# Performance work log

Hardware: AMD Instinct MI355X
Metric: run time of the kernel (lower is better)

Reference implementation:

```python
import math
import jax, jax.numpy as jnp
import numpy as np

B, CIN, COUT, K, T, S = 16, 512, 512, 3, 2048, 128


def setup_inputs() -> dict:
    key = jax.random.key(0)
    k1, k2, k3, k4 = jax.random.split(key, 4)
    x = jax.random.normal(k1, (B, CIN, T), dtype=jnp.float32)
    c_trg = jax.random.normal(k2, (B, S), dtype=jnp.float32)
    style_w = jax.random.normal(k3, (CIN, S), dtype=jnp.float32)  # EqualLinear weight (lr_mul=1)
    style_b = jnp.ones((CIN,), dtype=jnp.float32)  # bias_init=1
    conv_w = jax.random.normal(k4, (1, COUT, CIN, K), dtype=jnp.float32)
    return {"x": x, "c_trg": c_trg, "style_w": style_w, "style_b": style_b, "conv_w": conv_w}


def reference(x, c_trg, style_w, style_b, conv_w):
    b, cin, t = x.shape
    cout, k = conv_w.shape[1], conv_w.shape[3]
    lin_scale = 1.0 / math.sqrt(style_w.shape[1])  # EqualLinear scale, lr_mul=1
    # original forward calls style_linear twice -> s and b are the SAME value
    s = c_trg @ (style_w * lin_scale).T + style_b            # [B, Cin]
    s = s[:, None, :, None]                                   # [B, 1, Cin, 1]
    conv_scale = 1.0 / math.sqrt(cin * k ** 2)
    w = conv_scale * (conv_w * s + s)                         # [B, Cout, Cin, K]
    demod = jax.lax.rsqrt(jnp.sum(w * w, axis=(2, 3)) + 1e-8)  # [B, Cout]
    demod_mean = jnp.mean(w.reshape(b, cout, -1), axis=2)      # [B, Cout]
    w = (w - demod_mean[:, :, None, None]) * demod[:, :, None, None]
    pad = k // 2

    def conv1(xi, wi):  # xi [Cin, T], wi [Cout, Cin, K]
        return jax.lax.conv_general_dilated(
            xi[None], wi, window_strides=(1,), padding=[(pad, pad)],
            dimension_numbers=("NCH", "OIH", "NCH"))[0]

    out = jax.vmap(conv1)(x, w)  # [B, Cout, T]
    return out
```

## Files before the change

kernel.cpp:

```cpp
#include <hip/hip_runtime.h>
#include <hip/hip_bf16.h>
#include <stdint.h>

#define B_    16
#define CIN_  512
#define COUT_ 512
#define K_    3
#define T_    2048
#define S_    128
#define TP_   2064
#define CXP_  2050

#define LIN_SCALE  0.08838834764831845f
#define CONV_SCALE 0.014731391274719739f

typedef unsigned short u16;
typedef short s16x8 __attribute__((ext_vector_type(8)));
typedef float f32x4 __attribute__((ext_vector_type(4)));
typedef u16 u16x8 __attribute__((ext_vector_type(8)));

__device__ __forceinline__ u16 bf16r(float f) {
    uint32_t u = __float_as_uint(f);
    return (u16)((u + 0x7FFFu + ((u >> 16) & 1u)) >> 16);
}

#define GLDS16(gsrc, ldst) \
    __builtin_amdgcn_global_load_lds((__attribute__((address_space(1))) void*)(gsrc), \
                                     (__attribute__((address_space(3))) void*)(ldst), 16, 0, 0)

__global__ void k_style(const float* __restrict__ c_trg,
                        const float* __restrict__ style_w,
                        const float* __restrict__ style_b,
                        float* __restrict__ s_out) {
    int idx = blockIdx.x * 256 + threadIdx.x;
    int b = idx >> 9, i = idx & 511;
    const float4* c4 = reinterpret_cast<const float4*>(c_trg + b * S_);
    const float4* w4 = reinterpret_cast<const float4*>(style_w + (size_t)i * S_);
    float acc = 0.f;
#pragma unroll
    for (int j = 0; j < S_ / 4; ++j) {
        float4 a = c4[j], w = w4[j];
        acc += a.x * w.x + a.y * w.y + a.z * w.z + a.w * w.w;
    }
    s_out[idx] = acc * LIN_SCALE + style_b[i];
}

__global__ void k_wsum(const float* __restrict__ conv_w,
                       float* __restrict__ W1, float* __restrict__ W2) {
    int idx = blockIdx.x * 256 + threadIdx.x;
    const float* wr = conv_w + (size_t)idx * 3;
    float a0 = wr[0] + 1.f, a1 = wr[1] + 1.f, a2 = wr[2] + 1.f;
    W1[idx] = a0 + a1 + a2;
    W2[idx] = a0 * a0 + a1 * a1 + a2 * a2;
}

__global__ void k_stats2(const float* __restrict__ s,
                         const float* __restrict__ W1, const float* __restrict__ W2,
                         float* __restrict__ alpha, float* __restrict__ beta) {
    int bo = blockIdx.x;
    int b = bo >> 9, o = bo & 511;
    const float* sb = s + b * CIN_;
    const float* w1 = W1 + (size_t)o * CIN_;
    const float* w2 = W2 + (size_t)o * CIN_;
    int l = threadIdx.x;
    float sum = 0.f, sq = 0.f;
#pragma unroll
    for (int r = 0; r < 8; ++r) {
        float sv = sb[l + r * 64];
        sum += sv * w1[l + r * 64];
        sq  += sv * sv * w2[l + r * 64];
    }
#pragma unroll
    for (int off = 32; off; off >>= 1) { sum += __shfl_down(sum, off); sq += __shfl_down(sq, off); }
    if (l == 0) {
        float mean  = CONV_SCALE * sum * (1.0f / (CIN_ * K_));
        float demod = rsqrtf(CONV_SCALE * CONV_SCALE * sq + 1e-8f);
        alpha[bo] = demod * CONV_SCALE;
        beta[bo]  = demod * mean;
    }
}

__global__ void k_prep_w(const float* __restrict__ conv_w, u16* __restrict__ wpk) {
    int idx = blockIdx.x * 256 + threadIdx.x;
    int j    = idx & 7;
    int lane = (idx >> 3) & 63;
    int grp  = (idx >> 9) & 7;
    int rest = idx >> 12;
    int tap  = rest % 3;
    int so   = rest / 3;
    int step = so & 15, ob = so >> 4;
    int o = ob * 128 + grp * 16 + (lane & 15);
    int i = step * 32 + (lane >> 4) * 8 + j;
    wpk[idx] = bf16r(conv_w[((size_t)o * CIN_ + i) * 3 + tap]);
}

__global__ void k_ytrans(const float* __restrict__ x, const float* __restrict__ s,
                         u16* __restrict__ ybf,
                         float* __restrict__ cxp, float* __restrict__ cyp) {
    int t = blockIdx.x * 256 + threadIdx.x;
    int oct = blockIdx.y, b = blockIdx.z;
    const float* xb = x + ((size_t)(b * CIN_ + oct * 8)) * T_ + t;
    const float* sb = s + b * CIN_ + oct * 8;
    float ax = 0.f, ay = 0.f;
    u16x8 pv;
#pragma unroll
    for (int j = 0; j < 8; ++j) {
        float xv = xb[(size_t)j * T_];
        float yv = sb[j] * xv;
        ax += xv; ay += yv;
        pv[j] = bf16r(yv);
    }
    *(u16x8*)(ybf + (((size_t)(b * 64 + oct)) * TP_ + t + 8) * 8) = pv;
    atomicAdd(&cxp[b * CXP_ + t + 1], ax);
    atomicAdd(&cyp[b * CXP_ + t + 1], ay);
    if (blockIdx.x == 0 && threadIdx.x < 8) {
        u16x8 z = {0, 0, 0, 0, 0, 0, 0, 0};
        *(u16x8*)(ybf + (((size_t)(b * 64 + oct)) * TP_ + threadIdx.x) * 8) = z;
    }
    if (blockIdx.x == 7 && threadIdx.x >= 248) {
        u16x8 z = {0, 0, 0, 0, 0, 0, 0, 0};
        *(u16x8*)(ybf + (((size_t)(b * 64 + oct)) * TP_ + 2056 + (threadIdx.x - 248)) * 8) = z;
    }
}

__global__ __launch_bounds__(256) void k_conv(
    const u16* __restrict__ wpk, const u16* __restrict__ ybf,
    const float* __restrict__ alpha, const float* __restrict__ beta,
    const float* __restrict__ cxp, const float* __restrict__ cyp,
    float* __restrict__ out) {

    __shared__ __align__(16) char smem[33792];

    const int tid  = threadIdx.x;
    const int lane = tid & 63;
    const int w    = tid >> 6;
    const int wr   = w >> 1, wc = w & 1;
    const int t0   = blockIdx.x * 128;
    const int ob   = blockIdx.y;
    const int b    = blockIdx.z;

    f32x4 acc[4][4] = {};

    const char* wsrc  = (const char*)wpk + (size_t)(ob * 16) * 24576 + (w * 6) * 1024 + lane * 16;
    const char* ybase = (const char*)ybf + ((size_t)b * 64) * (TP_ * 16);

    const int as_lane = wr * 4096 + lane * 16;
    const int xs_lane = 24576 + (lane >> 4) * 2304 + ((lane & 15) + 7) * 16 + wc * 1024;

    for (int step = 0; step < 16; ++step) {
        __syncthreads();
#pragma unroll
        for (int r = 0; r < 6; ++r)
            GLDS16(wsrc + (size_t)step * 24576 + r * 1024, smem + (w * 6 + r) * 1024);
#pragma unroll
        for (int rb = w; rb < 9; rb += 4) {
            int c  = rb * 64 + lane;
            int g  = c / 144;
            int rr = c - g * 144;
            GLDS16(ybase + ((size_t)((step * 4 + g) * TP_) + t0 + rr) * 16,
                   smem + 24576 + rb * 1024);
        }
        __syncthreads();

#pragma unroll
        for (int tap = 0; tap < 3; ++tap) {
            s16x8 af[4], bq[4];
#pragma unroll
            for (int m = 0; m < 4; ++m)
                af[m] = *(const s16x8*)(smem + tap * 8192 + as_lane + m * 1024);
#pragma unroll
            for (int n = 0; n < 4; ++n)
                bq[n] = *(const s16x8*)(smem + xs_lane + tap * 16 + n * 256);
#pragma unroll
            for (int m = 0; m < 4; ++m)
#pragma unroll
                for (int n = 0; n < 4; ++n)
                    acc[m][n] = __builtin_amdgcn_mfma_f32_16x16x32_bf16(af[m], bq[n], acc[m][n], 0, 0, 0);
        }
    }

    const int lr = lane >> 4, lc = lane & 15;
    const int o0 = ob * 128 + wr * 64;
    const int tw = t0 + wc * 64;
    const float* al  = alpha + b * COUT_ + o0;
    const float* be  = beta  + b * COUT_ + o0;
    const float* cxb = cxp + b * CXP_;
    const float* cyb = cyp + b * CXP_;
    float* op = out + ((size_t)(b * COUT_ + o0)) * T_;

#pragma unroll
    for (int n = 0; n < 4; ++n) {
        int t = tw + n * 16 + lc;
        float cx3 = cxb[t] + cxb[t + 1] + cxb[t + 2];
        float cy3 = cyb[t] + cyb[t + 1] + cyb[t + 2];
#pragma unroll
        for (int m = 0; m < 4; ++m)
#pragma unroll
            for (int q = 0; q < 4; ++q) {
                int o = m * 16 + lr * 4 + q;
                op[(size_t)o * T_ + t] = al[o] * (acc[m][n][q] + cy3) - be[o] * cx3;
            }
    }
}

extern "C" void kernel_launch(void* const* d_in, const int* in_sizes, int n_in,
                              void* d_out, int out_size, void* d_ws, size_t ws_size,
                              hipStream_t stream) {
    const float* x       = (const float*)d_in[0];
    const float* c_trg   = (const float*)d_in[1];
    const float* style_w = (const float*)d_in[2];
    const float* style_b = (const float*)d_in[3];
    const float* conv_w  = (const float*)d_in[4];
    float* out = (float*)d_out;
    float* ws  = (float*)d_ws;

    float* s_buf = ws;
    float* alpha = ws + 8192;
    float* beta  = ws + 16384;
    float* cxp   = ws + 24576;
    float* cyp   = ws + 57376;
    float* W1    = ws + 90176;
    float* W2    = ws + 352320;
    u16*   wpk   = (u16*)(ws + 614464);
    u16*   ybf   = (u16*)(ws + 1007680);

    hipMemsetAsync(cxp, 0, (size_t)2 * CXP_ * B_ * sizeof(float), stream);

    k_style <<<dim3((B_ * CIN_) / 256), 256, 0, stream>>>(c_trg, style_w, style_b, s_buf);
    k_wsum  <<<dim3((COUT_ * CIN_) / 256), 256, 0, stream>>>(conv_w, W1, W2);
    k_prep_w<<<dim3((COUT_ * CIN_ * K_) / 256), 256, 0, stream>>>(conv_w, wpk);
    k_stats2<<<dim3(B_ * COUT_), 64, 0, stream>>>(s_buf, W1, W2, alpha, beta);
    k_ytrans<<<dim3(T_ / 256, CIN_ / 8, B_), 256, 0, stream>>>(x, s_buf, ybf, cxp, cyp);
    k_conv  <<<dim3(T_ / 128, COUT_ / 128, B_), 256, 0, stream>>>(wpk, ybf, alpha, beta, cxp, cyp, out);
}
```

Baseline: 226.2 us.

## Triple-buffer conv GEMM with async LDS loads, fuse stats kernels, coarsen ytrans

The conv kernel grows to 512 threads with a 128x256 tile and a three-stage LDS ring filled by global_load_lds, using vmcnt waits instead of full syncthreads, so global loads overlap MFMA work. It also raises wave priority around the MFMA loop and remaps block indices across the grid. The separate weight-sum and stats kernels are merged into one per-output-channel kernel that handles all batches from shared memory. The y-transform kernel handles eight channel groups per thread, which cuts atomic additions on the column sums eightfold. The costs are higher LDS use per block and fewer resident blocks.

After: 186.3 us. 17.6% less time.

```diff
diff --git a/kernel.cpp b/kernel.cpp
--- a/kernel.cpp
+++ b/kernel.cpp
@@ -11,6 +11,11 @@
 #define TP_   2064
 #define CXP_  2050
 
+#define ASZ   24576
+#define BSZ   17408
+#define BUFSZ (ASZ + BSZ)
+#define NBUF  3
+
 #define LIN_SCALE  0.08838834764831845f
 #define CONV_SCALE 0.014731391274719739f
 
@@ -27,6 +32,9 @@
 #define GLDS16(gsrc, ldst) \
     __builtin_amdgcn_global_load_lds((__attribute__((address_space(1))) void*)(gsrc), \
                                      (__attribute__((address_space(3))) void*)(ldst), 16, 0, 0)
+#define GLDS4(gsrc, ldst) \
+    __builtin_amdgcn_global_load_lds((__attribute__((address_space(1))) void*)(gsrc), \
+                                     (__attribute__((address_space(3))) void*)(ldst), 4, 0, 0)
 
 __global__ void k_style(const float* __restrict__ c_trg,
                         const float* __restrict__ style_w,
@@ -45,38 +53,51 @@
     s_out[idx] = acc * LIN_SCALE + style_b[i];
 }
 
-__global__ void k_wsum(const float* __restrict__ conv_w,
-                       float* __restrict__ W1, float* __restrict__ W2) {
-    int idx = blockIdx.x * 256 + threadIdx.x;
-    const float* wr = conv_w + (size_t)idx * 3;
+__global__ __launch_bounds__(256) void k_stats3(
+    const float* __restrict__ s, const float* __restrict__ conv_w,
+    float* __restrict__ alpha, float* __restrict__ beta) {
+    __shared__ float sl[B_ * CIN_];
+    __shared__ float red[4][32];
+    __shared__ float tot[32];
+    const int tid = threadIdx.x, o = blockIdx.x;
+    const int lane = tid & 63, wid = tid >> 6;
+#pragma unroll
+    for (int r = 0; r < 8; ++r) {
+        float4 v = *(const float4*)(s + r * 1024 + tid * 4);
+        *(float4*)(sl + r * 1024 + tid * 4) = v;
+    }
+    __syncthreads();
+    const float* wr = conv_w + (size_t)o * (CIN_ * K_) + tid * 6;
     float a0 = wr[0] + 1.f, a1 = wr[1] + 1.f, a2 = wr[2] + 1.f;
-    W1[idx] = a0 + a1 + a2;
-    W2[idx] = a0 * a0 + a1 * a1 + a2 * a2;
-}
-
-__global__ void k_stats2(const float* __restrict__ s,
-                         const float* __restrict__ W1, const float* __restrict__ W2,
-                         float* __restrict__ alpha, float* __restrict__ beta) {
-    int bo = blockIdx.x;
-    int b = bo >> 9, o = bo & 511;
-    const float* sb = s + b * CIN_;
-    const float* w1 = W1 + (size_t)o * CIN_;
-    const float* w2 = W2 + (size_t)o * CIN_;
-    int l = threadIdx.x;
-    float sum = 0.f, sq = 0.f;
-#pragma unroll
-    for (int r = 0; r < 8; ++r) {
-        float sv = sb[l + r * 64];
-        sum += sv * w1[l + r * 64];
-        sq  += sv * sv * w2[l + r * 64];
-    }
-#pragma unroll
-    for (int off = 32; off; off >>= 1) { sum += __shfl_down(sum, off); sq += __shfl_down(sq, off); }
-    if (l == 0) {
-        float mean  = CONV_SCALE * sum * (1.0f / (CIN_ * K_));
-        float demod = rsqrtf(CONV_SCALE * CONV_SCALE * sq + 1e-8f);
-        alpha[bo] = demod * CONV_SCALE;
-        beta[bo]  = demod * mean;
+    float b0 = wr[3] + 1.f, b1 = wr[4] + 1.f, b2 = wr[5] + 1.f;
+    float W1a = a0 + a1 + a2, W2a = a0 * a0 + a1 * a1 + a2 * a2;
+    float W1b = b0 + b1 + b2, W2b = b0 * b0 + b1 * b1 + b2 * b2;
+    int i = tid * 2;
+    float psum[16], psq[16];
+#pragma unroll
+    for (int b = 0; b < 16; ++b) {
+        float sa = sl[b * CIN_ + i], sb2 = sl[b * CIN_ + i + 1];
+        psum[b] = sa * W1a + sb2 * W1b;
+        psq[b]  = sa * sa * W2a + sb2 * sb2 * W2b;
+    }
+#pragma unroll
+    for (int off = 32; off; off >>= 1)
+#pragma unroll
+        for (int b = 0; b < 16; ++b) {
+            psum[b] += __shfl_down(psum[b], off);
+            psq[b]  += __shfl_down(psq[b], off);
+        }
+    if (lane == 0)
+#pragma unroll
+        for (int b = 0; b < 16; ++b) { red[wid][b] = psum[b]; red[wid][16 + b] = psq[b]; }
+    __syncthreads();
+    if (tid < 32) tot[tid] = red[0][tid] + red[1][tid] + red[2][tid] + red[3][tid];
+    __syncthreads();
+    if (tid < 16) {
+        float mean  = CONV_SCALE * tot[tid] * (1.0f / (CIN_ * K_));
+        float demod = rsqrtf(CONV_SCALE * CONV_SCALE * tot[16 + tid] + 1e-8f);
+        alpha[tid * COUT_ + o] = demod * CONV_SCALE;
+        beta[tid * COUT_ + o]  = demod * mean;
     }
 }
 
@@ -97,87 +118,119 @@
 __global__ void k_ytrans(const float* __restrict__ x, const float* __restrict__ s,
                          u16* __restrict__ ybf,
                          float* __restrict__ cxp, float* __restrict__ cyp) {
-    int t = blockIdx.x * 256 + threadIdx.x;
-    int oct = blockIdx.y, b = blockIdx.z;
-    const float* xb = x + ((size_t)(b * CIN_ + oct * 8)) * T_ + t;
-    const float* sb = s + b * CIN_ + oct * 8;
+    int tid = threadIdx.x;
+    int t = blockIdx.x * 256 + tid;
+    int og = blockIdx.y, b = blockIdx.z;
     float ax = 0.f, ay = 0.f;
-    u16x8 pv;
-#pragma unroll
-    for (int j = 0; j < 8; ++j) {
-        float xv = xb[(size_t)j * T_];
-        float yv = sb[j] * xv;
-        ax += xv; ay += yv;
-        pv[j] = bf16r(yv);
-    }
-    *(u16x8*)(ybf + (((size_t)(b * 64 + oct)) * TP_ + t + 8) * 8) = pv;
+#pragma unroll
+    for (int o8 = 0; o8 < 8; ++o8) {
+        int oct = og * 8 + o8;
+        const float* xb = x + ((size_t)(b * CIN_ + oct * 8)) * T_ + t;
+        const float* sb = s + b * CIN_ + oct * 8;
+        u16x8 pv;
+#pragma unroll
+        for (int j = 0; j < 8; ++j) {
+            float xv = xb[(size_t)j * T_];
+            float yv = sb[j] * xv;
+            ax += xv; ay += yv;
+            pv[j] = bf16r(yv);
+        }
+        *(u16x8*)(ybf + (((size_t)(b * 64 + oct)) * TP_ + t + 8) * 8) = pv;
+    }
     atomicAdd(&cxp[b * CXP_ + t + 1], ax);
     atomicAdd(&cyp[b * CXP_ + t + 1], ay);
-    if (blockIdx.x == 0 && threadIdx.x < 8) {
+    if (blockIdx.x == 0 && tid < 64) {
         u16x8 z = {0, 0, 0, 0, 0, 0, 0, 0};
-        *(u16x8*)(ybf + (((size_t)(b * 64 + oct)) * TP_ + threadIdx.x) * 8) = z;
-    }
-    if (blockIdx.x == 7 && threadIdx.x >= 248) {
-        u16x8 z = {0, 0, 0, 0, 0, 0, 0, 0};
-        *(u16x8*)(ybf + (((size_t)(b * 64 + oct)) * TP_ + 2056 + (threadIdx.x - 248)) * 8) = z;
-    }
-}
-
-__global__ __launch_bounds__(256) void k_conv(
+        int oct = og * 8 + (tid >> 3);
+        *(u16x8*)(ybf + (((size_t)(b * 64 + oct)) * TP_ + (tid & 7)) * 8) = z;
+        *(u16x8*)(ybf + (((size_t)(b * 64 + oct)) * TP_ + 2056 + (tid & 7)) * 8) = z;
+    }
+}
+
+__global__ __launch_bounds__(512) void k_conv(
     const u16* __restrict__ wpk, const u16* __restrict__ ybf,
     const float* __restrict__ alpha, const float* __restrict__ beta,
     const float* __restrict__ cxp, const float* __restrict__ cyp,
     float* __restrict__ out) {
 
-    __shared__ __align__(16) char smem[33792];
+    __shared__ __align__(16) char smem[NBUF * BUFSZ];
 
     const int tid  = threadIdx.x;
     const int lane = tid & 63;
     const int w    = tid >> 6;
-    const int wr   = w >> 1, wc = w & 1;
-    const int t0   = blockIdx.x * 128;
-    const int ob   = blockIdx.y;
-    const int b    = blockIdx.z;
+    const int wr   = w >> 2, wc = w & 3;
+
+    const int bid = blockIdx.x;
+    const int wg  = (bid & 7) * 64 + (bid >> 3);
+    const int b   = wg >> 5;
+    const int ob  = (wg >> 3) & 3;
+    const int t0  = (wg & 7) * 256;
+
+    const char* abase = (const char*)wpk + (size_t)ob * 393216;
+    const int aoff0 = (3 * w + 0) * 1024 + lane * 16;
+    const int aoff1 = (3 * w + 1) * 1024 + lane * 16;
+    const int aoff2 = (3 * w + 2) * 1024 + lane * 16;
+
+    const char* ybase = (const char*)ybf + ((size_t)b * 64) * (TP_ * 16);
+    const int c0 = tid, c1 = 512 + tid;
+    const int g0 = c0 / 272, rr0 = c0 - g0 * 272;
+    const int g1 = c1 / 272, rr1 = c1 - g1 * 272;
+    const size_t boff0 = ((size_t)g0 * TP_ + t0 + rr0) * 16;
+    const size_t boff1 = ((size_t)g1 * TP_ + t0 + rr1) * 16;
+    const int rowf = 1024 + ((tid & 255) >> 2);
+    const size_t boff2 = ((size_t)3 * TP_ + t0 + (rowf - 816)) * 16 + (tid & 3) * 4;
+    const int bdst0 = ASZ + c0 * 16, bdst1 = ASZ + c1 * 16;
+    const int bdst2 = ASZ + 16384 + (tid & 255) * 4;
+
+    const int as_lane = wr * 4096 + lane * 16;
+    const int xs_lane = ASZ + (lane >> 4) * 4352 + ((lane & 15) + 7) * 16 + wc * 1024;
 
     f32x4 acc[4][4] = {};
 
-    const char* wsrc  = (const char*)wpk + (size_t)(ob * 16) * 24576 + (w * 6) * 1024 + lane * 16;
-    const char* ybase = (const char*)ybf + ((size_t)b * 64) * (TP_ * 16);
-
-    const int as_lane = wr * 4096 + lane * 16;
-    const int xs_lane = 24576 + (lane >> 4) * 2304 + ((lane & 15) + 7) * 16 + wc * 1024;
-
-    for (int step = 0; step < 16; ++step) {
-        __syncthreads();
-#pragma unroll
-        for (int r = 0; r < 6; ++r)
-            GLDS16(wsrc + (size_t)step * 24576 + r * 1024, smem + (w * 6 + r) * 1024);
-#pragma unroll
-        for (int rb = w; rb < 9; rb += 4) {
-            int c  = rb * 64 + lane;
-            int g  = c / 144;
-            int rr = c - g * 144;
-            GLDS16(ybase + ((size_t)((step * 4 + g) * TP_) + t0 + rr) * 16,
-                   smem + 24576 + rb * 1024);
-        }
-        __syncthreads();
-
+#define STAGE(s)                                                             \
+    do {                                                                     \
+        char* dst = smem + ((s) % NBUF) * BUFSZ;                             \
+        const char* asrc = abase + (size_t)(s) * ASZ;                        \
+        const char* bsrc = ybase + (size_t)(s) * (4 * TP_ * 16);             \
+        GLDS16(asrc + aoff0, dst + aoff0);                                   \
+        GLDS16(asrc + aoff1, dst + aoff1);                                   \
+        GLDS16(asrc + aoff2, dst + aoff2);                                   \
+        GLDS16(bsrc + boff0, dst + bdst0);                                   \
+        GLDS16(bsrc + boff1, dst + bdst1);                                   \
+        GLDS4 (bsrc + boff2, dst + bdst2);                                   \
+    } while (0)
+
+    STAGE(0);
+    STAGE(1);
+
+#pragma unroll
+    for (int s = 0; s < 16; ++s) {
+        if (s < 15) asm volatile("s_waitcnt vmcnt(6)" ::: "memory");
+        else        asm volatile("s_waitcnt vmcnt(0)" ::: "memory");
+        __builtin_amdgcn_s_barrier();
+        asm volatile("" ::: "memory");
+        if (s + 2 < 16) STAGE(s + 2);
+
+        const char* base = smem + (s % NBUF) * BUFSZ;
+        __builtin_amdgcn_s_setprio(1);
 #pragma unroll
         for (int tap = 0; tap < 3; ++tap) {
             s16x8 af[4], bq[4];
 #pragma unroll
             for (int m = 0; m < 4; ++m)
-                af[m] = *(const s16x8*)(smem + tap * 8192 + as_lane + m * 1024);
+                af[m] = *(const s16x8*)(base + tap * 8192 + as_lane + m * 1024);
 #pragma unroll
             for (int n = 0; n < 4; ++n)
-                bq[n] = *(const s16x8*)(smem + xs_lane + tap * 16 + n * 256);
+                bq[n] = *(const s16x8*)(base + xs_lane + tap * 16 + n * 256);
 #pragma unroll
             for (int m = 0; m < 4; ++m)
 #pragma unroll
                 for (int n = 0; n < 4; ++n)
                     acc[m][n] = __builtin_amdgcn_mfma_f32_16x16x32_bf16(af[m], bq[n], acc[m][n], 0, 0, 0);
         }
-    }
+        __builtin_amdgcn_s_setprio(0);
+    }
+#undef STAGE
 
     const int lr = lane >> 4, lc = lane & 15;
     const int o0 = ob * 128 + wr * 64;
@@ -219,17 +272,14 @@
     float* beta  = ws + 16384;
     float* cxp   = ws + 24576;
     float* cyp   = ws + 57376;
-    float* W1    = ws + 90176;
-    float* W2    = ws + 352320;
-    u16*   wpk   = (u16*)(ws + 614464);
-    u16*   ybf   = (u16*)(ws + 1007680);
+    u16*   wpk   = (u16*)(ws + 90176);
+    u16*   ybf   = (u16*)(ws + 483392);
 
     hipMemsetAsync(cxp, 0, (size_t)2 * CXP_ * B_ * sizeof(float), stream);
 
     k_style <<<dim3((B_ * CIN_) / 256), 256, 0, stream>>>(c_trg, style_w, style_b, s_buf);
-    k_wsum  <<<dim3((COUT_ * CIN_) / 256), 256, 0, stream>>>(conv_w, W1, W2);
     k_prep_w<<<dim3((COUT_ * CIN_ * K_) / 256), 256, 0, stream>>>(conv_w, wpk);
-    k_stats2<<<dim3(B_ * COUT_), 64, 0, stream>>>(s_buf, W1, W2, alpha, beta);
-    k_ytrans<<<dim3(T_ / 256, CIN_ / 8, B_), 256, 0, stream>>>(x, s_buf, ybf, cxp, cyp);
-    k_conv  <<<dim3(T_ / 128, COUT_ / 128, B_), 256, 0, stream>>>(wpk, ybf, alpha, beta, cxp, cyp, out);
-}
+    k_stats3<<<dim3(COUT_), 256, 0, stream>>>(s_buf, conv_w, alpha, beta);
+    k_ytrans<<<dim3(T_ / 256, 8, B_), 256, 0, stream>>>(x, s_buf, ybf, cxp, cyp);
+    k_conv  <<<dim3(512), 512, 0, stream>>>(wpk, ybf, alpha, beta, cxp, cyp, out);
+}
```
